# Kernel optimization log

Hardware: AMD Instinct MI355X
Metric: run time of the kernel (lower is better)

## Reference

```python
import jax, jax.numpy as jnp
import numpy as np


def _bag_mean(idx, table):
    # F.embedding_bag(mode='mean', padding_idx=last row): padding entries are
    # excluded from both the sum and the count. idx: [B, S, K]
    pad = table.shape[0] - 1
    mask = (idx != pad)[..., None].astype(table.dtype)          # [B,S,K,1]
    emb = table[idx] * mask                                      # [B,S,K,D]
    cnt = mask.sum(axis=-2)                                      # [B,S,1]
    s = emb.sum(axis=-2)                                         # [B,S,D]
    return jnp.where(cnt > 0, s / jnp.maximum(cnt, 1.0), 0.0)


def _subgraph_parts(qq, ques_table, skill_table, diff_table, area_table,
                    ques2skill, ques2diff, ques2area):
    qe = ques_table[qq]                                          # [B,S,D]
    sk = _bag_mean(ques2skill[qq], skill_table)                  # [B,S,D]
    df = diff_table[ques2diff[qq][..., 0]]                       # [B,S,D]
    ar = area_table[ques2area[qq][..., 0]]                       # [B,S,D]
    return qe, sk, df, ar


def reference(q, a, next_q, ques_table, skill_table, diff_table, area_table,
              ques2skill, ques2diff, ques2area, Wq, bq):
    # ---- get_subgraph_embedding (non-JunYi path) ----
    qe, sk, df, ar = _subgraph_parts(q, ques_table, skill_table, diff_table,
                                     area_table, ques2skill, ques2diff, ques2area)
    q_emb = (qe + sk + df + ar) / 4.0

    nqe, nsk, ndf, nar = _subgraph_parts(next_q, ques_table, skill_table,
                                         diff_table, area_table, ques2skill,
                                         ques2diff, ques2area)
    nq_emb = (nqe + nsk + ndf + nar) / 4.0
    # faithful to source: the averaging line for next_q is applied twice
    nq_emb = (nq_emb + nsk + ndf + nar) / 4.0

    q_emb = q_emb @ Wq.T + bq
    nq_emb = nq_emb @ Wq.T + bq

    # ---- Fusion_Module: answer==1 keeps first half, answer==0 keeps second ----
    af = a[..., None].astype(q_emb.dtype)                        # [B,S,1]
    input_emb = jnp.concatenate([q_emb * af, q_emb * (1.0 - af)], axis=-1)

    return jnp.concatenate([input_emb, nq_emb], axis=-1)        # [B,S,3D]


def setup_inputs() -> dict:
    key = jax.random.key(0)
    ks = jax.random.split(key, 12)
    B, S, D = 16, 2048, 128
    NQ, NS, ND, NA, K = 200001, 2001, 100, 50, 8
    return {
        "q": jax.random.randint(ks[0], (B, S), 0, NQ - 1),
        "a": jax.random.randint(ks[1], (B, S), 0, 2),
        "next_q": jax.random.randint(ks[2], (B, S), 0, NQ - 1),
        "ques_table": jax.random.normal(ks[3], (NQ, D), jnp.float32),
        "skill_table": jax.random.normal(ks[4], (NS, D), jnp.float32),
        "diff_table": jax.random.normal(ks[5], (ND, D), jnp.float32),
        "area_table": jax.random.normal(ks[6], (NA, D), jnp.float32),
        "ques2skill": jax.random.randint(ks[7], (NQ, K), 0, NS),
        "ques2diff": jax.random.randint(ks[8], (NQ, 1), 0, ND),
        "ques2area": jax.random.randint(ks[9], (NQ, 1), 0, NA),
        "Wq": jax.random.normal(ks[10], (D, D), jnp.float32) / np.sqrt(D),
        "bq": jax.random.normal(ks[11], (D,), jnp.float32) * 0.01,
    }
```

## Files before the change

### kernel.cpp

```cpp
#include <hip/hip_runtime.h>
#include <hip/hip_bf16.h>

typedef float  f32x4  __attribute__((ext_vector_type(4)));
typedef short  s16x8  __attribute__((ext_vector_type(8)));

#define PIN_LOADS() asm volatile("" ::: "memory")

__device__ __forceinline__ unsigned short f2bf(float f) {
    unsigned int u = __float_as_uint(f);
    unsigned int rnd = 0x7fffu + ((u >> 16) & 1u);
    return (unsigned short)((u + rnd) >> 16);
}

__device__ __forceinline__ void bf8_fma(const s16x8 v, float s, f32x4& a0, f32x4& a1) {
    const uint4 u = *(const uint4*)&v;
    a0[0] += s * __uint_as_float(u.x << 16);
    a0[1] += s * __uint_as_float(u.x & 0xffff0000u);
    a0[2] += s * __uint_as_float(u.y << 16);
    a0[3] += s * __uint_as_float(u.y & 0xffff0000u);
    a1[0] += s * __uint_as_float(u.z << 16);
    a1[1] += s * __uint_as_float(u.z & 0xffff0000u);
    a1[2] += s * __uint_as_float(u.w << 16);
    a1[3] += s * __uint_as_float(u.w & 0xffff0000u);
}

__global__ __launch_bounds__(256)
void h2kt_prep(const float* __restrict__ Wq,
               const float* __restrict__ skill, const float* __restrict__ diff,
               const float* __restrict__ area,
               const int* __restrict__ q, const int* __restrict__ next_q,
               const int* __restrict__ a_arr,
               const int* __restrict__ q2s, const int* __restrict__ q2d,
               const int* __restrict__ q2a,
               const float* __restrict__ ques_table,
               unsigned short* __restrict__ Wqb,
               unsigned short* __restrict__ T2,
               int* __restrict__ desc,
               int pad_idx)
{
    const int bid = blockIdx.x, tid = threadIdx.x;

    if (bid < 8) {
        const int s  = bid * 256 + tid;
        const int f  = s >> 6, sl = s & 63;
        const int jt = f >> 2, kt = f & 3;
        const int row = jt * 16 + (sl & 15);
        const int col = kt * 32 + (sl >> 4) * 8;
        const float4 w0 = *(const float4*)(Wq + row * 128 + col);
        const float4 w1 = *(const float4*)(Wq + row * 128 + col + 4);
        s16x8 v;
        v[0] = (short)f2bf(w0.x); v[1] = (short)f2bf(w0.y);
        v[2] = (short)f2bf(w0.z); v[3] = (short)f2bf(w0.w);
        v[4] = (short)f2bf(w1.x); v[5] = (short)f2bf(w1.y);
        v[6] = (short)f2bf(w1.z); v[7] = (short)f2bf(w1.w);
        *(s16x8*)(Wqb + (size_t)s * 8) = v;
    } else if (bid < 42) {
        const int lane = tid & 63;
        const int cl = lane & 15, grp = lane >> 4;
        const int row16 = ((bid - 8) * 4 + (tid >> 6)) * 16;
        if (row16 > 2150) return;

        int srow = row16 + cl;
        if (srow > 2150) srow = 2150;
        const float* src = (srow < 2001) ? skill + (size_t)srow * 128
                         : (srow < 2101) ? diff + (size_t)(srow - 2001) * 128
                                         : area + (size_t)(srow - 2101) * 128;
        s16x8 afr[4];
        #pragma unroll
        for (int kt = 0; kt < 4; ++kt) {
            const float4 v0 = *(const float4*)(src + kt * 32 + grp * 8);
            const float4 v1 = *(const float4*)(src + kt * 32 + grp * 8 + 4);
            s16x8 v;
            v[0] = (short)f2bf(v0.x); v[1] = (short)f2bf(v0.y);
            v[2] = (short)f2bf(v0.z); v[3] = (short)f2bf(v0.w);
            v[4] = (short)f2bf(v1.x); v[5] = (short)f2bf(v1.y);
            v[6] = (short)f2bf(v1.z); v[7] = (short)f2bf(v1.w);
            afr[kt] = v;
        }
        #pragma unroll
        for (int jt = 0; jt < 8; ++jt) {
            f32x4 acc = {0.f, 0.f, 0.f, 0.f};
            #pragma unroll
            for (int kt = 0; kt < 4; ++kt) {
                const float* wp = Wq + (jt * 16 + cl) * 128 + kt * 32 + grp * 8;
                const float4 w0 = *(const float4*)(wp);
                const float4 w1 = *(const float4*)(wp + 4);
                s16x8 bf;
                bf[0] = (short)f2bf(w0.x); bf[1] = (short)f2bf(w0.y);
                bf[2] = (short)f2bf(w0.z); bf[3] = (short)f2bf(w0.w);
                bf[4] = (short)f2bf(w1.x); bf[5] = (short)f2bf(w1.y);
                bf[6] = (short)f2bf(w1.z); bf[7] = (short)f2bf(w1.w);
                acc = __builtin_amdgcn_mfma_f32_16x16x32_bf16(afr[kt], bf, acc, 0, 0, 0);
            }
            #pragma unroll
            for (int r = 0; r < 4; ++r) {
                const int orow = row16 + grp * 4 + r;
                if (orow < 2151) T2[(size_t)orow * 128 + jt * 16 + cl] = f2bf(acc[r]);
            }
        }
    } else {
        const int g = (bid - 42) * 256 + tid;
        const int p = g & 32767;
        const bool isnq = (g >= 32768);
        const int qq = isnq ? next_q[p] : q[p];
        const int4 s03 = *(const int4*)(q2s + (size_t)qq * 8);
        const int4 s47 = *(const int4*)(q2s + (size_t)qq * 8 + 4);
        const int di = q2d[qq];
        const int ai = q2a[qq];
        const int av = isnq ? 1 : a_arr[p];
        int4* d = (int4*)(desc + (size_t)g * 12);
        d[0] = make_int4(qq, s03.x, s03.y, s03.z);
        d[1] = make_int4(s03.w, s47.x, s47.y, s47.z);
        d[2] = make_int4(s47.w, 2001 + di, 2101 + ai, av);

        const f32x4* qp = (const f32x4*)(ques_table + (size_t)qq * 128);
        f32x4 acc = qp[0];
        #pragma unroll
        for (int i = 1; i < 8; ++i) acc += qp[i];
        asm volatile("" :: "v"(acc[0]), "v"(acc[1]), "v"(acc[2]), "v"(acc[3]));
    }
}

__global__ __launch_bounds__(256, 4)
void h2kt_fused(const int* __restrict__ desc,
                const float* __restrict__ ques_table,
                const unsigned short* __restrict__ T2,
                const unsigned short* __restrict__ Wqb,
                const float* __restrict__ bq,
                float* __restrict__ out,
                int pad_idx)
{
    __shared__ __align__(16) unsigned short Q[16 * 136];
    __shared__ __align__(16) float          D[16 * 132];

    const int tid  = threadIdx.x;
    const int w    = tid >> 6;
    const int lane = tid & 63;
    const int cl   = lane & 15;
    const int grp  = lane >> 4;
    const int r2   = lane >> 5;
    const int c    = lane & 31;
    const int g0   = blockIdx.x * 16;
    const int base = g0 & 32767;
    const bool isnq = (g0 >= 32768);
    const float wq_ = isnq ? 0.0625f : 0.25f;
    const float wr_ = isnq ? 0.3125f : 0.25f;

    const int myrow = w * 4 + grp;

    const int qq0 = desc[(size_t)(g0 + w * 4 + 0 + r2) * 12];
    const int qq1 = desc[(size_t)(g0 + w * 4 + 2 + r2) * 12];
    const int4* P = (const int4*)(desc + (size_t)(g0 + myrow) * 12);
    const int4 i0 = P[0], i1 = P[1], i2 = P[2];

    const f32x4 qv0 = *(const f32x4*)(ques_table + (size_t)qq0 * 128 + c * 4);
    const f32x4 qv1 = *(const f32x4*)(ques_table + (size_t)qq1 * 128 + c * 4);

    const int sa[8] = {i0.y, i0.z, i0.w, i1.x, i1.y, i1.z, i1.w, i2.x};
    const int av = i2.w;

    s16x8 t[10];
    #pragma unroll
    for (int i = 0; i < 8; ++i)
        t[i] = *(const s16x8*)(T2 + (size_t)sa[i] * 128 + cl * 8);
    t[8] = *(const s16x8*)(T2 + (size_t)i2.y * 128 + cl * 8);
    t[9] = *(const s16x8*)(T2 + (size_t)i2.z * 128 + cl * 8);
    PIN_LOADS();

    {
        ushort4 o;
        o.x = f2bf(wq_ * qv0[0]); o.y = f2bf(wq_ * qv0[1]);
        o.z = f2bf(wq_ * qv0[2]); o.w = f2bf(wq_ * qv0[3]);
        *(ushort4*)(Q + (size_t)(w * 4 + 0 + r2) * 136 + c * 4) = o;
        o.x = f2bf(wq_ * qv1[0]); o.y = f2bf(wq_ * qv1[1]);
        o.z = f2bf(wq_ * qv1[2]); o.w = f2bf(wq_ * qv1[3]);
        *(ushort4*)(Q + (size_t)(w * 4 + 2 + r2) * 136 + c * 4) = o;
    }

    __syncthreads();

    s16x8 afr[4];
    #pragma unroll
    for (int kt = 0; kt < 4; ++kt)
        afr[kt] = *(const s16x8*)(Q + (size_t)cl * 136 + kt * 32 + grp * 8);

    #pragma unroll
    for (int jt2 = 0; jt2 < 2; ++jt2) {
        const int jt = w * 2 + jt2;
        f32x4 acc = {0.f, 0.f, 0.f, 0.f};
        #pragma unroll
        for (int kt = 0; kt < 4; ++kt) {
            const s16x8 bf = *(const s16x8*)(Wqb + ((size_t)(jt * 4 + kt) * 64 + lane) * 8);
            acc = __builtin_amdgcn_mfma_f32_16x16x32_bf16(afr[kt], bf, acc, 0, 0, 0);
        }
        #pragma unroll
        for (int r = 0; r < 4; ++r)
            D[(size_t)(grp * 4 + r) * 132 + jt * 16 + cl] = acc[r];
    }

    int cnt = 0;
    #pragma unroll
    for (int i = 0; i < 8; ++i) cnt += (sa[i] != pad_idx);
    const float cs = cnt > 0 ? wr_ / (float)cnt : 0.f;

    f32x4 rA = {0,0,0,0}, rB = {0,0,0,0};
    #pragma unroll
    for (int i = 0; i < 8; ++i) bf8_fma(t[i], (sa[i] != pad_idx) ? cs : 0.f, rA, rB);
    bf8_fma(t[8], wr_, rA, rB);
    bf8_fma(t[9], wr_, rA, rB);

    __syncthreads();

    const f32x4 bq0 = *(const f32x4*)(bq + cl * 8);
    const f32x4 bq1 = *(const f32x4*)(bq + cl * 8 + 4);
    const f32x4 z = {0.f, 0.f, 0.f, 0.f};
    {
        const f32x4 d0 = *(const f32x4*)(D + (size_t)myrow * 132 + cl * 8);
        const f32x4 d1 = *(const f32x4*)(D + (size_t)myrow * 132 + cl * 8 + 4);
        const f32x4 v0 = d0 + rA + bq0;
        const f32x4 v1 = d1 + rB + bq1;
        const size_t orow = (size_t)(base + myrow);
        if (!isnq) {
            const bool on = (av != 0);
            *(f32x4*)(out + orow * 384 + cl * 8)           = on ? v0 : z;
            *(f32x4*)(out + orow * 384 + cl * 8 + 4)       = on ? v1 : z;
            *(f32x4*)(out + orow * 384 + 128 + cl * 8)     = on ? z : v0;
            *(f32x4*)(out + orow * 384 + 128 + cl * 8 + 4) = on ? z : v1;
        } else {
            *(f32x4*)(out + orow * 384 + 256 + cl * 8)     = v0;
            *(f32x4*)(out + orow * 384 + 256 + cl * 8 + 4) = v1;
        }
    }
}

extern "C" void kernel_launch(void* const* d_in, const int* in_sizes, int n_in,
                              void* d_out, int out_size, void* d_ws, size_t ws_size,
                              hipStream_t stream) {
    const int*   q          = (const int*)d_in[0];
    const int*   a          = (const int*)d_in[1];
    const int*   next_q     = (const int*)d_in[2];
    const float* ques_table = (const float*)d_in[3];
    const float* skill_tab  = (const float*)d_in[4];
    const float* diff_tab   = (const float*)d_in[5];
    const float* area_tab   = (const float*)d_in[6];
    const int*   q2s        = (const int*)d_in[7];
    const int*   q2d        = (const int*)d_in[8];
    const int*   q2a        = (const int*)d_in[9];
    const float* Wq         = (const float*)d_in[10];
    const float* bq         = (const float*)d_in[11];
    float* out = (float*)d_out;

    const int NS = in_sizes[4] / 128;
    const int pad_idx = NS - 1;

    int*            descp = (int*)d_ws;
    unsigned short* Wqb   = (unsigned short*)((char*)d_ws + (size_t)65536 * 48);
    unsigned short* T2    = Wqb + (size_t)2048 * 8;

    h2kt_prep<<<298, 256, 0, stream>>>(Wq, skill_tab, diff_tab, area_tab,
                                       q, next_q, a, q2s, q2d, q2a, ques_table,
                                       Wqb, T2, descp, pad_idx);
    h2kt_fused<<<4096, 256, 0, stream>>>(descp, ques_table, T2, Wqb, bq, out, pad_idx);
}
```

Baseline: 40.43 us.

## Pre-gather scaled bf16 question embeddings into linear buffer in prep kernel

The prep kernel gains 1024 extra blocks that gather each question's ques_table row, scale it by the path weight, convert it to bf16 and write it into a contiguous workspace buffer Qlin. The fused kernel then loads its MFMA A-fragments straight from Qlin, which removes the random fp32 gathers, the LDS staging buffer and a __syncthreads. The old prefetch loop that only warmed ques_table rows is dropped. In exchange there is an extra 16 MB global write and read round trip through Qlin and a larger prep launch.

```diff
diff --git a/kernel.cpp b/kernel.cpp
--- a/kernel.cpp
+++ b/kernel.cpp
@@ -36,6 +36,7 @@
                unsigned short* __restrict__ Wqb,
                unsigned short* __restrict__ T2,
                int* __restrict__ desc,
+               unsigned short* __restrict__ Qlin,
                int pad_idx)
 {
     const int bid = blockIdx.x, tid = threadIdx.x;
@@ -98,7 +99,7 @@
                 if (orow < 2151) T2[(size_t)orow * 128 + jt * 16 + cl] = f2bf(acc[r]);
             }
         }
-    } else {
+    } else if (bid < 298) {
         const int g = (bid - 42) * 256 + tid;
         const int p = g & 32767;
         const bool isnq = (g >= 32768);
@@ -112,50 +113,65 @@
         d[0] = make_int4(qq, s03.x, s03.y, s03.z);
         d[1] = make_int4(s03.w, s47.x, s47.y, s47.z);
         d[2] = make_int4(s47.w, 2001 + di, 2101 + ai, av);
-
-        const f32x4* qp = (const f32x4*)(ques_table + (size_t)qq * 128);
-        f32x4 acc = qp[0];
-        #pragma unroll
-        for (int i = 1; i < 8; ++i) acc += qp[i];
-        asm volatile("" :: "v"(acc[0]), "v"(acc[1]), "v"(acc[2]), "v"(acc[3]));
+    } else {
+        const int t   = (bid - 298) * 256 + tid;
+        const int gr  = t >> 2;
+        const int qtr = t & 3;
+        const int p   = gr & 32767;
+        const bool isnq = (gr >= 32768);
+        const int qq  = (isnq ? next_q : q)[p];
+        const float wq_ = isnq ? 0.0625f : 0.25f;
+
+        const f32x4* src = (const f32x4*)(ques_table + (size_t)qq * 128 + qtr * 32);
+        f32x4 v[8];
+        #pragma unroll
+        for (int i = 0; i < 8; ++i) v[i] = src[i];
+        PIN_LOADS();
+
+        unsigned short* dst = Qlin + (size_t)gr * 128 + qtr * 32;
+        #pragma unroll
+        for (int i = 0; i < 4; ++i) {
+            s16x8 o;
+            #pragma unroll
+            for (int j = 0; j < 4; ++j) {
+                o[j]     = (short)f2bf(wq_ * v[2 * i][j]);
+                o[j + 4] = (short)f2bf(wq_ * v[2 * i + 1][j]);
+            }
+            *(s16x8*)(dst + i * 8) = o;
+        }
     }
 }
 
 __global__ __launch_bounds__(256, 4)
 void h2kt_fused(const int* __restrict__ desc,
-                const float* __restrict__ ques_table,
+                const unsigned short* __restrict__ Qlin,
                 const unsigned short* __restrict__ T2,
                 const unsigned short* __restrict__ Wqb,
                 const float* __restrict__ bq,
                 float* __restrict__ out,
                 int pad_idx)
 {
-    __shared__ __align__(16) unsigned short Q[16 * 136];
-    __shared__ __align__(16) float          D[16 * 132];
+    __shared__ __align__(16) float D[16 * 132];
 
     const int tid  = threadIdx.x;
     const int w    = tid >> 6;
     const int lane = tid & 63;
     const int cl   = lane & 15;
     const int grp  = lane >> 4;
-    const int r2   = lane >> 5;
-    const int c    = lane & 31;
     const int g0   = blockIdx.x * 16;
     const int base = g0 & 32767;
     const bool isnq = (g0 >= 32768);
-    const float wq_ = isnq ? 0.0625f : 0.25f;
     const float wr_ = isnq ? 0.3125f : 0.25f;
 
     const int myrow = w * 4 + grp;
 
-    const int qq0 = desc[(size_t)(g0 + w * 4 + 0 + r2) * 12];
-    const int qq1 = desc[(size_t)(g0 + w * 4 + 2 + r2) * 12];
+    s16x8 afr[4];
+    #pragma unroll
+    for (int kt = 0; kt < 4; ++kt)
+        afr[kt] = *(const s16x8*)(Qlin + (size_t)(g0 + cl) * 128 + kt * 32 + grp * 8);
+
     const int4* P = (const int4*)(desc + (size_t)(g0 + myrow) * 12);
     const int4 i0 = P[0], i1 = P[1], i2 = P[2];
-
-    const f32x4 qv0 = *(const f32x4*)(ques_table + (size_t)qq0 * 128 + c * 4);
-    const f32x4 qv1 = *(const f32x4*)(ques_table + (size_t)qq1 * 128 + c * 4);
-
     const int sa[8] = {i0.y, i0.z, i0.w, i1.x, i1.y, i1.z, i1.w, i2.x};
     const int av = i2.w;
 
@@ -166,23 +182,6 @@
     t[8] = *(const s16x8*)(T2 + (size_t)i2.y * 128 + cl * 8);
     t[9] = *(const s16x8*)(T2 + (size_t)i2.z * 128 + cl * 8);
     PIN_LOADS();
-
-    {
-        ushort4 o;
-        o.x = f2bf(wq_ * qv0[0]); o.y = f2bf(wq_ * qv0[1]);
-        o.z = f2bf(wq_ * qv0[2]); o.w = f2bf(wq_ * qv0[3]);
-        *(ushort4*)(Q + (size_t)(w * 4 + 0 + r2) * 136 + c * 4) = o;
-        o.x = f2bf(wq_ * qv1[0]); o.y = f2bf(wq_ * qv1[1]);
-        o.z = f2bf(wq_ * qv1[2]); o.w = f2bf(wq_ * qv1[3]);
-        *(ushort4*)(Q + (size_t)(w * 4 + 2 + r2) * 136 + c * 4) = o;
-    }
-
-    __syncthreads();
-
-    s16x8 afr[4];
-    #pragma unroll
-    for (int kt = 0; kt < 4; ++kt)
-        afr[kt] = *(const s16x8*)(Q + (size_t)cl * 136 + kt * 32 + grp * 8);
 
     #pragma unroll
     for (int jt2 = 0; jt2 < 2; ++jt2) {
@@ -253,12 +252,13 @@
     const int NS = in_sizes[4] / 128;
     const int pad_idx = NS - 1;
 
-    int*            descp = (int*)d_ws;
-    unsigned short* Wqb   = (unsigned short*)((char*)d_ws + (size_t)65536 * 48);
+    unsigned short* Qlin  = (unsigned short*)d_ws;
+    int*            descp = (int*)((char*)d_ws + (size_t)65536 * 256);
+    unsigned short* Wqb   = (unsigned short*)((char*)descp + (size_t)65536 * 48);
     unsigned short* T2    = Wqb + (size_t)2048 * 8;
 
-    h2kt_prep<<<298, 256, 0, stream>>>(Wq, skill_tab, diff_tab, area_tab,
-                                       q, next_q, a, q2s, q2d, q2a, ques_table,
-                                       Wqb, T2, descp, pad_idx);
-    h2kt_fused<<<4096, 256, 0, stream>>>(descp, ques_table, T2, Wqb, bq, out, pad_idx);
-}
+    h2kt_prep<<<1322, 256, 0, stream>>>(Wq, skill_tab, diff_tab, area_tab,
+                                        q, next_q, a, q2s, q2d, q2a, ques_table,
+                                        Wqb, T2, descp, Qlin, pad_idx);
+    h2kt_fused<<<4096, 256, 0, stream>>>(descp, Qlin, T2, Wqb, bq, out, pad_idx);
+}
```

Result: slower. 49.38 us (median of 2 runs) (+22.1%).
